# Kernel optimization log

Measured on AMD Instinct MI355X. Metric: run time of the kernel, lower is better.

The kernel has to match this reference:

```python
import jax, jax.numpy as jnp
import numpy as np

B, T, D = 32, 2048, 512
BATCH_SIZE = 32  # config.batch_size: number of MVN draws


def setup_inputs() -> dict:
    key = jax.random.key(0)
    k1, k2 = jax.random.split(key)
    x = jax.random.normal(k1, (B, T, D), dtype=jnp.float32)
    z = jax.random.normal(k2, (BATCH_SIZE, D), dtype=jnp.float32)  # standard-normal noise for reparameterized MVN draw
    return {"x": x, "z": z}


def reference(x, z):
    # mean over batch and time -> [D]
    mean = jnp.mean(x, axis=(0, 1))
    # per-batch covariance over time axis, then mean over batch -> [D, D]
    t = x.shape[1]
    xc = x - jnp.mean(x, axis=1, keepdims=True)
    # sum over b and t fused: equals mean_b( xc_b^T xc_b / (t-1) )
    cov = jnp.einsum('btd,bte->de', xc, xc) / ((t - 1) * x.shape[0])
    # multivariate normal draw via Cholesky reparameterization:
    # sample = mean + z @ L^T, L L^T = cov
    L = jnp.linalg.cholesky(cov)
    return mean + z @ L.T
```

## Files before the change

### kernel.cpp

```cpp
#include <hip/hip_runtime.h>

#define Dn 512
#define Bn 32
#define Tn 2048
#define BT 65536
#define NCHUNK 64
#define CHUNK_K 1024

typedef unsigned short u16;
typedef __attribute__((ext_vector_type(8))) short short8;
typedef __attribute__((ext_vector_type(4))) float floatx4;

__device__ __forceinline__ u16 f2bf(float f) {
    unsigned u = __float_as_uint(f);
    unsigned r = (u + 0x7FFFu + ((u >> 16) & 1u)) >> 16;
    return (u16)r;
}
__device__ __forceinline__ float bf2f(u16 s) { return __uint_as_float(((unsigned)s) << 16); }

#define GLL(gp, sp) __builtin_amdgcn_global_load_lds( \
    (const __attribute__((address_space(1))) void*)(gp), \
    (__attribute__((address_space(3))) void*)(sp), 16, 0, 0)

#define RLF(x, L) __uint_as_float(__builtin_amdgcn_readlane(__float_as_uint(x), (L)))

#define REP64(X) X(0) X(1) X(2) X(3) X(4) X(5) X(6) X(7) X(8) X(9) X(10) X(11) X(12) X(13) X(14) X(15) \
    X(16) X(17) X(18) X(19) X(20) X(21) X(22) X(23) X(24) X(25) X(26) X(27) X(28) X(29) X(30) X(31) \
    X(32) X(33) X(34) X(35) X(36) X(37) X(38) X(39) X(40) X(41) X(42) X(43) X(44) X(45) X(46) X(47) \
    X(48) X(49) X(50) X(51) X(52) X(53) X(54) X(55) X(56) X(57) X(58) X(59) X(60) X(61) X(62) X(63)
#define REPJH1(OP, K) OP(K,0) OP(K,1) OP(K,2) OP(K,3) OP(K,4) OP(K,5) OP(K,6) OP(K,7) OP(K,8) OP(K,9) \
    OP(K,10) OP(K,11) OP(K,12) OP(K,13) OP(K,14) OP(K,15) OP(K,16) OP(K,17) OP(K,18) OP(K,19) \
    OP(K,20) OP(K,21) OP(K,22) OP(K,23) OP(K,24) OP(K,25) OP(K,26) OP(K,27) OP(K,28) OP(K,29) \
    OP(K,30) OP(K,31)
#define REPJH2(OP, K) OP(K,32) OP(K,33) OP(K,34) OP(K,35) OP(K,36) OP(K,37) OP(K,38) OP(K,39) \
    OP(K,40) OP(K,41) OP(K,42) OP(K,43) OP(K,44) OP(K,45) OP(K,46) OP(K,47) OP(K,48) OP(K,49) \
    OP(K,50) OP(K,51) OP(K,52) OP(K,53) OP(K,54) OP(K,55) OP(K,56) OP(K,57) OP(K,58) OP(K,59) \
    OP(K,60) OP(K,61) OP(K,62) OP(K,63)
#define REPQA(OP, C) OP(C,0,0,0) OP(C,1,0,1) OP(C,2,0,2) OP(C,3,0,3) OP(C,4,1,0) OP(C,5,1,1) OP(C,6,1,2) OP(C,7,1,3) \
    OP(C,8,2,0) OP(C,9,2,1) OP(C,10,2,2) OP(C,11,2,3) OP(C,12,3,0) OP(C,13,3,1) OP(C,14,3,2) OP(C,15,3,3)
#define REPQB(OP, C) OP(C,16,4,0) OP(C,17,4,1) OP(C,18,4,2) OP(C,19,4,3) OP(C,20,5,0) OP(C,21,5,1) OP(C,22,5,2) OP(C,23,5,3) \
    OP(C,24,6,0) OP(C,25,6,1) OP(C,26,6,2) OP(C,27,6,3) OP(C,28,7,0) OP(C,29,7,1) OP(C,30,7,2) OP(C,31,7,3)
#define REPQC(OP, C) OP(C,32,8,0) OP(C,33,8,1) OP(C,34,8,2) OP(C,35,8,3) OP(C,36,9,0) OP(C,37,9,1) OP(C,38,9,2) OP(C,39,9,3) \
    OP(C,40,10,0) OP(C,41,10,1) OP(C,42,10,2) OP(C,43,10,3) OP(C,44,11,0) OP(C,45,11,1) OP(C,46,11,2) OP(C,47,11,3)
#define REPQD(OP, C) OP(C,48,12,0) OP(C,49,12,1) OP(C,50,12,2) OP(C,51,12,3) OP(C,52,13,0) OP(C,53,13,1) OP(C,54,13,2) OP(C,55,13,3) \
    OP(C,56,14,0) OP(C,57,14,1) OP(C,58,14,2) OP(C,59,14,3) OP(C,60,15,0) OP(C,61,15,1) OP(C,62,15,2) OP(C,63,15,3)
#define REPQ(OP, C) REPQA(OP, C) REPQB(OP, C) REPQC(OP, C) REPQD(OP, C)
#define REPW(OP) OP(0,0,1,2,3) OP(1,4,5,6,7) OP(2,8,9,10,11) OP(3,12,13,14,15) OP(4,16,17,18,19) \
    OP(5,20,21,22,23) OP(6,24,25,26,27) OP(7,28,29,30,31) OP(8,32,33,34,35) OP(9,36,37,38,39) \
    OP(10,40,41,42,43) OP(11,44,45,46,47) OP(12,48,49,50,51) OP(13,52,53,54,55) OP(14,56,57,58,59) \
    OP(15,60,61,62,63)

__global__ __launch_bounds__(256) void k_zero(float* __restrict__ mu) {
    floatx4 z = {0.f, 0.f, 0.f, 0.f};
    ((floatx4*)mu)[blockIdx.x * 256 + threadIdx.x] = z;
}

__global__ __launch_bounds__(256) void k_transpose(const float* __restrict__ x,
                                                   u16* __restrict__ Xt,
                                                   float* __restrict__ mu) {
    int tt = blockIdx.x;
    int dt = blockIdx.y;
    int b  = blockIdx.z;
    __shared__ u16 sT[64][68];
    int tid = threadIdx.x;
    int row = tid >> 4;
    int c4  = (tid & 15) * 4;
    const float* src = x + ((long)b * Tn + (long)tt * 64) * Dn + dt * 64;
#pragma unroll
    for (int q = 0; q < 4; q++) {
        int r = row + q * 16;
        floatx4 v = *(const floatx4*)(src + (long)r * Dn + c4);
        sT[c4 + 0][r] = f2bf(v[0]);
        sT[c4 + 1][r] = f2bf(v[1]);
        sT[c4 + 2][r] = f2bf(v[2]);
        sT[c4 + 3][r] = f2bf(v[3]);
    }
    __syncthreads();
    int drow = tid >> 3;
    int koff = (tid & 7) * 8;
    long kout = (long)b * Tn + (long)tt * 64 + koff;
#pragma unroll
    for (int p = 0; p < 2; p++) {
        int dr = drow + p * 32;
        u16 tmp[8];
        float s = 0.f;
#pragma unroll
        for (int j = 0; j < 8; j++) {
            tmp[j] = sT[dr][koff + j];
            s += bf2f(tmp[j]);
        }
        *(short8*)(Xt + (long)(dt * 64 + dr) * BT + kout) = *(short8*)tmp;
        s += __shfl_down(s, 4, 64);
        s += __shfl_down(s, 2, 64);
        s += __shfl_down(s, 1, 64);
        if ((tid & 7) == 0) atomicAdd(mu + b * 512 + dt * 64 + dr, s);
    }
}

__global__ __launch_bounds__(256, 3) void k_gram(const u16* __restrict__ Xt,
                                                 float* __restrict__ partial) {
    int chunk = blockIdx.x;
    int pos = blockIdx.y;
    int di = (pos < 4) ? 0 : (pos < 7) ? 1 : (pos < 9) ? 2 : 3;
    int start = di * 4 - (di * (di - 1)) / 2;
    int ei = di + (pos - start);
    int d0 = di * 128, e0 = ei * 128;

    __shared__ u16 sA[128 * 32];
    __shared__ u16 sB[128 * 32];
    int tid = threadIdx.x;
    int w = tid >> 6, l = tid & 63;
    int wm = w & 1, wn = w >> 1;
    long kbase = (long)chunk * CHUNK_K;
    int srow = w * 16 + (l >> 2);
    int sk = (l & 3) * 8;
    const u16* gA0 = Xt + (long)(d0 + srow) * BT + kbase + sk;
    const u16* gA1 = gA0 + 64l * BT;
    const u16* gB0 = Xt + (long)(e0 + srow) * BT + kbase + sk;
    const u16* gB1 = gB0 + 64l * BT;
    u16* sA0 = sA + (w * 16) * 32;
    u16* sA1 = sA0 + 64 * 32;
    u16* sB0 = sB + (w * 16) * 32;
    u16* sB1 = sB0 + 64 * 32;
    int m = l & 15, g = l >> 4;
    const u16* fA = sA + (wm * 64 + m) * 32 + g * 8;
    const u16* fB = sB + (wn * 64 + m) * 32 + g * 8;

    floatx4 acc[4][4] = {};
    for (int kk = 0; kk < CHUNK_K; kk += 32) {
        GLL(gA0 + kk, sA0);
        GLL(gA1 + kk, sA1);
        GLL(gB0 + kk, sB0);
        GLL(gB1 + kk, sB1);
        __syncthreads();
        short8 af[4], bfv[4];
#pragma unroll
        for (int i = 0; i < 4; i++) af[i] = *(const short8*)(fA + i * 16 * 32);
#pragma unroll
        for (int j = 0; j < 4; j++) bfv[j] = *(const short8*)(fB + j * 16 * 32);
#pragma unroll
        for (int i = 0; i < 4; i++)
#pragma unroll
            for (int j = 0; j < 4; j++)
                acc[i][j] = __builtin_amdgcn_mfma_f32_16x16x32_bf16(af[i], bfv[j], acc[i][j], 0, 0, 0);
        __syncthreads();
    }
    float* P = partial + (long)chunk * (512l * 512);
    int col = l & 15, rowg = (l >> 4) * 4;
#pragma unroll
    for (int i = 0; i < 4; i++)
#pragma unroll
        for (int j = 0; j < 4; j++) {
            int rr = d0 + wm * 64 + i * 16 + rowg;
            int cc = e0 + wn * 64 + j * 16 + col;
#pragma unroll
            for (int r = 0; r < 4; r++) P[(long)(rr + r) * 512 + cc] = acc[i][j][r];
        }
}

__global__ __launch_bounds__(256) void k_assemble(const float* __restrict__ partial,
                                                  const float* __restrict__ mu,
                                                  float* __restrict__ A) {
    int d = blockIdx.y;
    int e = blockIdx.x * 256 + threadIdx.x;
    int bd = d >> 7, be = e >> 7;
    long idx = (bd <= be) ? ((long)d * 512 + e) : ((long)e * 512 + d);
    float s = 0.f;
#pragma unroll
    for (int c = 0; c < NCHUNK; c++) s += partial[c * (512l * 512) + idx];
    float msum = 0.f;
#pragma unroll
    for (int b = 0; b < 32; b++) msum += mu[b * 512 + d] * mu[b * 512 + e];
    A[(long)d * 512 + e] = (s - msum * (1.0f / Tn)) * (1.0f / ((Tn - 1.0f) * Bn));
}

__global__ __launch_bounds__(64, 1) void k_chol_panel(float* __restrict__ A, int kb) {
    const int k0 = kb * 64;
    const int lane = threadIdx.x;

    const float* Dr = A + (long)(k0 + lane) * 512 + k0;
#define LDV(Q,A0,A1,A2,A3) floatx4 v##Q = *(const floatx4*)(Dr + 4*(Q));
    REPW(LDV)
#undef LDV
#define DECR(C,M,Mq,e) float r##M = v##Mq[(e)];
    REPQ(DECR, 0)
#undef DECR

    float vinv = 0.f;
#define SH1(K,J) float t##J = ((J) > (K)) ? RLF(lik, J) : 0.0f;
#define FM1(K,J) if ((J) > (K)) r##J = fmaf(nlik, t##J, r##J);
#define STEP(K) { float akk = RLF(r##K, K); float sd = sqrtf(akk); \
                  float inv = 1.0f / sd; float lik = (lane == (K)) ? sd : r##K * inv; \
                  r##K = lik; if (lane == (K)) vinv = inv; float nlik = -lik; \
                  { REPJH1(SH1, K) REPJH1(FM1, K) } { REPJH2(SH1, K) REPJH2(FM1, K) } }
    REP64(STEP)
#undef STEP
#undef FM1
#undef SH1

    if (blockIdx.x == 0) {
        float* W = A + (long)(k0 + lane) * 512 + k0;
#define STW(Q,A0,A1,A2,A3) { floatx4 w; w[0]=r##A0; w[1]=r##A1; w[2]=r##A2; w[3]=r##A3; \
                             *(floatx4*)(W + 4*(Q)) = w; }
        REPW(STW)
#undef STW
        return;
    }

    int rbase = k0 + 64 + (blockIdx.x - 1) * 64;
    const float* R = A + (long)(rbase + lane) * 512 + k0;
#define LDA(Q,A0,A1,A2,A3) floatx4 u##Q = *(const floatx4*)(R + 4*(Q));
    REPW(LDA)
#undef LDA
#define DECA(C,M,Mq,e) float a##M = u##Mq[(e)];
    REPQ(DECA, 0)
#undef DECA
#define TRL(C,M,Mq,e) float t##M = ((M) < (C)) ? RLF(r##M, C) : 0.0f;
#define TFM(C,M,Mq,e) if ((M) < (C)) acc##e = fmaf(a##M, t##M, acc##e);
#define TSTEP(C) { float acc0 = 0.f, acc1 = 0.f, acc2 = 0.f, acc3 = 0.f; \
                   { REPQA(TRL, C) REPQA(TFM, C) } { REPQB(TRL, C) REPQB(TFM, C) } \
                   { REPQC(TRL, C) REPQC(TFM, C) } { REPQD(TRL, C) REPQD(TFM, C) } \
                   float invC = RLF(vinv, C); \
                   a##C = (a##C - ((acc0 + acc1) + (acc2 + acc3))) * invC; }
    REP64(TSTEP)
#undef TSTEP
#undef TFM
#undef TRL

    float* Wr = A + (long)(rbase + lane) * 512 + k0;
#define STA(Q,A0,A1,A2,A3) { floatx4 w; w[0]=a##A0; w[1]=a##A1; w[2]=a##A2; w[3]=a##A3; \
                             *(floatx4*)(Wr + 4*(Q)) = w; }
    REPW(STA)
#undef STA
}

__global__ __launch_bounds__(256) void k_chol_update(float* __restrict__ A, int kb) {
    int k0 = kb * 64, base = k0 + 64;
    int idx = blockIdx.x, ti = 0;
    while (idx > ti) { idx -= ti + 1; ti++; }
    int tj = idx;
    int r0 = base + ti * 64, c0 = base + tj * 64;
    __shared__ float sI[64][65];
    __shared__ float sJ[64][65];
    int tid = threadIdx.x;
    int row = tid >> 4, c4 = (tid & 15) * 4;
#pragma unroll
    for (int q = 0; q < 4; q++) {
        int rr = row + q * 16;
        *(floatx4*)&sI[rr][c4] = *(const floatx4*)(A + (long)(r0 + rr) * 512 + k0 + c4);
        *(floatx4*)&sJ[rr][c4] = *(const floatx4*)(A + (long)(c0 + rr) * 512 + k0 + c4);
    }
    __syncthreads();
    int ri = (tid >> 4) * 4, cj = (tid & 15) * 4;
    float acc[4][4] = {};
    for (int k = 0; k < 64; k += 4) {
        floatx4 av[4], bv[4];
#pragma unroll
        for (int ii = 0; ii < 4; ii++) av[ii] = *(const floatx4*)&sI[ri + ii][k];
#pragma unroll
        for (int jj = 0; jj < 4; jj++) bv[jj] = *(const floatx4*)&sJ[cj + jj][k];
#pragma unroll
        for (int ii = 0; ii < 4; ii++)
#pragma unroll
            for (int jj = 0; jj < 4; jj++)
#pragma unroll
                for (int q = 0; q < 4; q++)
                    acc[ii][jj] = fmaf(av[ii][q], bv[jj][q], acc[ii][jj]);
    }
#pragma unroll
    for (int ii = 0; ii < 4; ii++) {
        float* dst = A + (long)(r0 + ri + ii) * 512 + c0 + cj;
        floatx4 old = *(const floatx4*)dst;
#pragma unroll
        for (int jj = 0; jj < 4; jj++) old[jj] -= acc[ii][jj];
        *(floatx4*)dst = old;
    }
}

__global__ __launch_bounds__(512) void k_output(const float* __restrict__ z,
                                                const float* __restrict__ A,
                                                const float* __restrict__ mu,
                                                float* __restrict__ out) {
    int i = blockIdx.x, d = threadIdx.x;
    __shared__ float sz[512];
    sz[d] = z[(long)i * 512 + d];
    __syncthreads();
    float mean = 0.f;
#pragma unroll
    for (int b = 0; b < 32; b++) mean += mu[b * 512 + d];
    mean *= (1.0f / (32.0f * 2048.0f));
    const float* Lr = A + (long)d * 512;
    float acc = 0.f;
    int dmax = d + 1;
    int e4 = dmax & ~3;
    for (int e = 0; e < e4; e += 4) {
        floatx4 l = *(const floatx4*)(Lr + e);
        acc += l[0] * sz[e] + l[1] * sz[e + 1] + l[2] * sz[e + 2] + l[3] * sz[e + 3];
    }
    for (int e = e4; e < dmax; e++) acc += Lr[e] * sz[e];
    out[(long)i * 512 + d] = mean + acc;
}

extern "C" void kernel_launch(void* const* d_in, const int* in_sizes, int n_in,
                              void* d_out, int out_size, void* d_ws, size_t ws_size,
                              hipStream_t stream) {
    const float* x = (const float*)d_in[0];
    const float* z = (const float*)d_in[1];
    float* out = (float*)d_out;
    char* ws = (char*)d_ws;
    u16* Xt = (u16*)ws;
    float* mu = (float*)(ws + 67108864);
    float* partial = (float*)(ws + 67108864 + 65536);
    float* A = (float*)(ws + 67108864 + 65536 + 67108864);

    k_zero<<<16, 256, 0, stream>>>(mu);
    k_transpose<<<dim3(32, 8, 32), 256, 0, stream>>>(x, Xt, mu);
    k_gram<<<dim3(NCHUNK, 10), 256, 0, stream>>>(Xt, partial);
    k_assemble<<<dim3(2, 512), 256, 0, stream>>>(partial, mu, A);
    for (int kb = 0; kb < 8; kb++) {
        int nb = 7 - kb;
        k_chol_panel<<<nb + 1, 64, 0, stream>>>(A, kb);
        int tiles = nb * (nb + 1) / 2;
        if (tiles > 0) k_chol_update<<<tiles, 256, 0, stream>>>(A, kb);
    }
    k_output<<<32, 512, 0, stream>>>(z, A, mu, out);
}
```

Before: 574.8 us.

## Fuse Cholesky panel factor, triangular solve and trailing update into one kernel

Merges the per-block panel factorization, triangular solve and trailing-matrix update into a single kernel per block column. Each update block redundantly refactors the 64x64 diagonal block and solves its own two panel rows in waves 0 and 1, keeping them in shared memory, so no separate panel launch and no global round trip are needed between panel and update. The final L is written to a separate buffer so that other blocks can keep reading the untouched A panel. This halves the number of serialized launches in the Cholesky loop, at the cost of repeating the diagonal factorization in every block.

Result: faster. 558.5 us (-2.8%).

```diff
diff --git a/kernel.cpp b/kernel.cpp
--- a/kernel.cpp
+++ b/kernel.cpp
@@ -174,46 +174,55 @@
     A[(long)d * 512 + e] = (s - msum * (1.0f / Tn)) * (1.0f / ((Tn - 1.0f) * Bn));
 }
 
-__global__ __launch_bounds__(64, 1) void k_chol_panel(float* __restrict__ A, int kb) {
+__global__ __launch_bounds__(256, 1) void k_chol_step(float* __restrict__ A,
+                                                      float* __restrict__ L,
+                                                      int kb) {
     const int k0 = kb * 64;
-    const int lane = threadIdx.x;
-
-    const float* Dr = A + (long)(k0 + lane) * 512 + k0;
+    const int tid = threadIdx.x;
+    const int lane = tid & 63;
+    const int wave = tid >> 6;
+    int idx = blockIdx.x, ti = 0;
+    while (idx > ti) { idx -= ti + 1; ti++; }
+    const int tj = idx;
+    const int row0 = k0 + 64 + ti * 64;
+    const int col0 = k0 + 64 + tj * 64;
+    __shared__ float sI[64 * 65];
+    __shared__ float sJ[64 * 65];
+
+    if (wave < 2) {
+        const float* Dr = A + (long)(k0 + lane) * 512 + k0;
 #define LDV(Q,A0,A1,A2,A3) floatx4 v##Q = *(const floatx4*)(Dr + 4*(Q));
-    REPW(LDV)
+        REPW(LDV)
 #undef LDV
 #define DECR(C,M,Mq,e) float r##M = v##Mq[(e)];
-    REPQ(DECR, 0)
+        REPQ(DECR, 0)
 #undef DECR
-
-    float vinv = 0.f;
+        float vinv = 0.f;
 #define SH1(K,J) float t##J = ((J) > (K)) ? RLF(lik, J) : 0.0f;
 #define FM1(K,J) if ((J) > (K)) r##J = fmaf(nlik, t##J, r##J);
 #define STEP(K) { float akk = RLF(r##K, K); float sd = sqrtf(akk); \
                   float inv = 1.0f / sd; float lik = (lane == (K)) ? sd : r##K * inv; \
                   r##K = lik; if (lane == (K)) vinv = inv; float nlik = -lik; \
                   { REPJH1(SH1, K) REPJH1(FM1, K) } { REPJH2(SH1, K) REPJH2(FM1, K) } }
-    REP64(STEP)
+        REP64(STEP)
 #undef STEP
 #undef FM1
 #undef SH1
-
-    if (blockIdx.x == 0) {
-        float* W = A + (long)(k0 + lane) * 512 + k0;
+        if (blockIdx.x == 0 && wave == 0) {
+            float* W = L + (long)(k0 + lane) * 512 + k0;
 #define STW(Q,A0,A1,A2,A3) { floatx4 w; w[0]=r##A0; w[1]=r##A1; w[2]=r##A2; w[3]=r##A3; \
                              *(floatx4*)(W + 4*(Q)) = w; }
-        REPW(STW)
+            REPW(STW)
 #undef STW
-        return;
-    }
-
-    int rbase = k0 + 64 + (blockIdx.x - 1) * 64;
-    const float* R = A + (long)(rbase + lane) * 512 + k0;
+        }
+
+        const int sbase = (wave == 0) ? row0 : col0;
+        const float* R = A + (long)(sbase + lane) * 512 + k0;
 #define LDA(Q,A0,A1,A2,A3) floatx4 u##Q = *(const floatx4*)(R + 4*(Q));
-    REPW(LDA)
+        REPW(LDA)
 #undef LDA
 #define DECA(C,M,Mq,e) float a##M = u##Mq[(e)];
-    REPQ(DECA, 0)
+        REPQ(DECA, 0)
 #undef DECA
 #define TRL(C,M,Mq,e) float t##M = ((M) < (C)) ? RLF(r##M, C) : 0.0f;
 #define TFM(C,M,Mq,e) if ((M) < (C)) acc##e = fmaf(a##M, t##M, acc##e);
@@ -222,63 +231,83 @@
                    { REPQC(TRL, C) REPQC(TFM, C) } { REPQD(TRL, C) REPQD(TFM, C) } \
                    float invC = RLF(vinv, C); \
                    a##C = (a##C - ((acc0 + acc1) + (acc2 + acc3))) * invC; }
-    REP64(TSTEP)
+        REP64(TSTEP)
 #undef TSTEP
 #undef TFM
 #undef TRL
-
-    float* Wr = A + (long)(rbase + lane) * 512 + k0;
+        float* sS = (wave == 0) ? sI : sJ;
+#define STS(Q,A0,A1,A2,A3) { floatx4 w; w[0]=a##A0; w[1]=a##A1; w[2]=a##A2; w[3]=a##A3; \
+                             *(floatx4*)(sS + lane * 65 + 4*(Q)) = w; }
+        REPW(STS)
+#undef STS
+        if (ti == tj && wave == 0) {
+            float* Wr = L + (long)(row0 + lane) * 512 + k0;
 #define STA(Q,A0,A1,A2,A3) { floatx4 w; w[0]=a##A0; w[1]=a##A1; w[2]=a##A2; w[3]=a##A3; \
                              *(floatx4*)(Wr + 4*(Q)) = w; }
-    REPW(STA)
+            REPW(STA)
 #undef STA
-}
-
-__global__ __launch_bounds__(256) void k_chol_update(float* __restrict__ A, int kb) {
-    int k0 = kb * 64, base = k0 + 64;
-    int idx = blockIdx.x, ti = 0;
-    while (idx > ti) { idx -= ti + 1; ti++; }
-    int tj = idx;
-    int r0 = base + ti * 64, c0 = base + tj * 64;
-    __shared__ float sI[64][65];
-    __shared__ float sJ[64][65];
-    int tid = threadIdx.x;
-    int row = tid >> 4, c4 = (tid & 15) * 4;
-#pragma unroll
-    for (int q = 0; q < 4; q++) {
-        int rr = row + q * 16;
-        *(floatx4*)&sI[rr][c4] = *(const floatx4*)(A + (long)(r0 + rr) * 512 + k0 + c4);
-        *(floatx4*)&sJ[rr][c4] = *(const floatx4*)(A + (long)(c0 + rr) * 512 + k0 + c4);
+        }
     }
     __syncthreads();
-    int ri = (tid >> 4) * 4, cj = (tid & 15) * 4;
-    float acc[4][4] = {};
-    for (int k = 0; k < 64; k += 4) {
-        floatx4 av[4], bv[4];
-#pragma unroll
-        for (int ii = 0; ii < 4; ii++) av[ii] = *(const floatx4*)&sI[ri + ii][k];
-#pragma unroll
-        for (int jj = 0; jj < 4; jj++) bv[jj] = *(const floatx4*)&sJ[cj + jj][k];
-#pragma unroll
-        for (int ii = 0; ii < 4; ii++)
-#pragma unroll
-            for (int jj = 0; jj < 4; jj++)
-#pragma unroll
-                for (int q = 0; q < 4; q++)
-                    acc[ii][jj] = fmaf(av[ii][q], bv[jj][q], acc[ii][jj]);
-    }
-#pragma unroll
-    for (int ii = 0; ii < 4; ii++) {
-        float* dst = A + (long)(r0 + ri + ii) * 512 + c0 + cj;
-        floatx4 old = *(const floatx4*)dst;
-#pragma unroll
-        for (int jj = 0; jj < 4; jj++) old[jj] -= acc[ii][jj];
-        *(floatx4*)dst = old;
-    }
+
+    {
+        int ri = (tid >> 4) * 4, cj = (tid & 15) * 4;
+        float acc[4][4] = {};
+        for (int k = 0; k < 64; k += 4) {
+            floatx4 av[4], bv[4];
+#pragma unroll
+            for (int ii = 0; ii < 4; ii++) av[ii] = *(const floatx4*)&sI[(ri + ii) * 65 + k];
+#pragma unroll
+            for (int jj = 0; jj < 4; jj++) bv[jj] = *(const floatx4*)&sJ[(cj + jj) * 65 + k];
+#pragma unroll
+            for (int ii = 0; ii < 4; ii++)
+#pragma unroll
+                for (int jj = 0; jj < 4; jj++)
+#pragma unroll
+                    for (int q = 0; q < 4; q++)
+                        acc[ii][jj] = fmaf(av[ii][q], bv[jj][q], acc[ii][jj]);
+        }
+#pragma unroll
+        for (int ii = 0; ii < 4; ii++) {
+            float* dst = A + (long)(row0 + ri + ii) * 512 + col0 + cj;
+            floatx4 old = *(const floatx4*)dst;
+#pragma unroll
+            for (int jj = 0; jj < 4; jj++) old[jj] -= acc[ii][jj];
+            *(floatx4*)dst = old;
+        }
+    }
+}
+
+__global__ __launch_bounds__(64, 1) void k_chol_last(const float* __restrict__ A,
+                                                     float* __restrict__ L) {
+    const int k0 = 7 * 64;
+    const int lane = threadIdx.x;
+    const float* Dr = A + (long)(k0 + lane) * 512 + k0;
+#define LDV(Q,A0,A1,A2,A3) floatx4 v##Q = *(const floatx4*)(Dr + 4*(Q));
+    REPW(LDV)
+#undef LDV
+#define DECR(C,M,Mq,e) float r##M = v##Mq[(e)];
+    REPQ(DECR, 0)
+#undef DECR
+#define SH1(K,J) float t##J = ((J) > (K)) ? RLF(lik, J) : 0.0f;
+#define FM1(K,J) if ((J) > (K)) r##J = fmaf(nlik, t##J, r##J);
+#define STEP(K) { float akk = RLF(r##K, K); float sd = sqrtf(akk); \
+                  float inv = 1.0f / sd; float lik = (lane == (K)) ? sd : r##K * inv; \
+                  r##K = lik; float nlik = -lik; \
+                  { REPJH1(SH1, K) REPJH1(FM1, K) } { REPJH2(SH1, K) REPJH2(FM1, K) } }
+    REP64(STEP)
+#undef STEP
+#undef FM1
+#undef SH1
+    float* W = L + (long)(k0 + lane) * 512 + k0;
+#define STW(Q,A0,A1,A2,A3) { floatx4 w; w[0]=r##A0; w[1]=r##A1; w[2]=r##A2; w[3]=r##A3; \
+                             *(floatx4*)(W + 4*(Q)) = w; }
+    REPW(STW)
+#undef STW
 }
 
 __global__ __launch_bounds__(512) void k_output(const float* __restrict__ z,
-                                                const float* __restrict__ A,
+                                                const float* __restrict__ L,
                                                 const float* __restrict__ mu,
                                                 float* __restrict__ out) {
     int i = blockIdx.x, d = threadIdx.x;
@@ -289,7 +318,7 @@
 #pragma unroll
     for (int b = 0; b < 32; b++) mean += mu[b * 512 + d];
     mean *= (1.0f / (32.0f * 2048.0f));
-    const float* Lr = A + (long)d * 512;
+    const float* Lr = L + (long)d * 512;
     float acc = 0.f;
     int dmax = d + 1;
     int e4 = dmax & ~3;
@@ -312,16 +341,16 @@
     float* mu = (float*)(ws + 67108864);
     float* partial = (float*)(ws + 67108864 + 65536);
     float* A = (float*)(ws + 67108864 + 65536 + 67108864);
+    float* Lmat = (float*)(ws + 67108864 + 65536 + 67108864 + 1048576);
 
     k_zero<<<16, 256, 0, stream>>>(mu);
     k_transpose<<<dim3(32, 8, 32), 256, 0, stream>>>(x, Xt, mu);
     k_gram<<<dim3(NCHUNK, 10), 256, 0, stream>>>(Xt, partial);
     k_assemble<<<dim3(2, 512), 256, 0, stream>>>(partial, mu, A);
-    for (int kb = 0; kb < 8; kb++) {
+    for (int kb = 0; kb < 7; kb++) {
         int nb = 7 - kb;
-        k_chol_panel<<<nb + 1, 64, 0, stream>>>(A, kb);
-        int tiles = nb * (nb + 1) / 2;
-        if (tiles > 0) k_chol_update<<<tiles, 256, 0, stream>>>(A, kb);
-    }
-    k_output<<<32, 512, 0, stream>>>(z, A, mu, out);
-}
+        k_chol_step<<<nb * (nb + 1) / 2, 256, 0, stream>>>(A, Lmat, kb);
+    }
+    k_chol_last<<<1, 64, 0, stream>>>(A, Lmat);
+    k_output<<<32, 512, 0, stream>>>(z, Lmat, mu, out);
+}
```
